# Optimization experiments

Hardware: AMD Instinct MI355X
Metric: run time of the kernel (lower is better)

The kernel has to match this reference:

```python
import jax, jax.numpy as jnp
import numpy as np
from jax import lax

# QKeras quantized_bits(8, 0, alpha=1, keep_negative=1):
#   delta = 2^-(bits-1) = 1/128, q(x) = clip(round(x*128), -128, 127)/128
QB_SCALE = 128.0
# QKeras quantized_relu(8, 0): q(x) = clip(round(x*256), 0, 255)/256
QR_SCALE = 256.0

def _ste(q, x):
    # straight-through estimator: forward = q(x), backward = identity
    return x + lax.stop_gradient(q - x)

def qbits(x):
    q = jnp.clip(jnp.round(x * QB_SCALE), -QB_SCALE, QB_SCALE - 1.0) / QB_SCALE
    return _ste(q, x)

def qrelu(x):
    q = jnp.clip(jnp.round(x * QR_SCALE), 0.0, QR_SCALE - 1.0) / QR_SCALE
    return _ste(q, x)


def setup_inputs() -> dict:
    key = jax.random.key(0)
    ks = jax.random.split(key, 9)
    B, C, F = 1000000, 16, 3
    dims = [C * F, 64, 32, 32]
    x = jax.random.normal(ks[0], (B, C, F), dtype=jnp.float32)
    def w(k, i, o):
        return jax.random.normal(k, (i, o), dtype=jnp.float32) * (0.5 / np.sqrt(i))
    inp = {"x": x}
    for li in range(3):
        inp[f"w{li+1}"] = w(ks[1 + 2 * li], dims[li], dims[li + 1])
        inp[f"b{li+1}"] = jax.random.normal(ks[2 + 2 * li], (dims[li + 1],), dtype=jnp.float32) * 0.05
    inp["wout"] = w(ks[7], dims[-1], 5)
    inp["bout"] = jax.random.normal(ks[8], (5,), dtype=jnp.float32) * 0.05
    return inp


def reference(x, w1, b1, w2, b2, w3, b3, wout, bout):
    h = x.reshape(x.shape[0], -1)  # Flatten: [B, 48]
    for w, b in ((w1, b1), (w2, b2), (w3, b3)):
        # QDense: fake-quantize kernel & bias, fp32 matmul, quantized_relu
        h = qrelu(h @ qbits(w) + qbits(b))
    return h @ wout + bout  # final float Dense -> logits [B, 5]
```

## Files before the change

kernel.cpp:

```cpp
#include <hip/hip_runtime.h>
#include <hip/hip_bf16.h>

typedef short  short8 __attribute__((ext_vector_type(8)));
typedef float  f32x4  __attribute__((ext_vector_type(4)));
typedef unsigned int u32;
typedef unsigned long long u64;
typedef unsigned short u16;

__device__ __forceinline__ u32 f2bf(float v) {
    u32 u = __float_as_uint(v);
    return (u + 0x7FFFu + ((u >> 16) & 1u)) >> 16;
}
__device__ __forceinline__ float qround128(float w) {
    float q = rintf(w * 128.0f);
    return fminf(fmaxf(q, -128.0f), 127.0f);
}
__device__ __forceinline__ u32 cvtpk(float a, float b) {
    __hip_bfloat162 h = __float22bfloat162_rn(make_float2(a, b));
    union { __hip_bfloat162 h; u32 u; } cv; cv.h = h; return cv.u;
}
__device__ __forceinline__ float q255(float v) {
    return fminf(fmaxf(rintf(v), 0.f), 255.f);
}
union FragU { short8 s; u32 u[4]; };
__device__ __forceinline__ short8 pack2(f32x4 a, f32x4 b) {
    FragU f;
    f.u[0] = cvtpk(q255(a[0]), q255(a[1]));
    f.u[1] = cvtpk(q255(a[2]), q255(a[3]));
    f.u[2] = cvtpk(q255(b[0]), q255(b[1]));
    f.u[3] = cvtpk(q255(b[2]), q255(b[3]));
    return f.s;
}
__device__ __forceinline__ f32x4 mfma16(short8 a, short8 b, f32x4 c) {
    return __builtin_amdgcn_mfma_f32_16x16x32_bf16(a, b, c, 0, 0, 0);
}


__global__ void prep(const float* __restrict__ w1, const float* __restrict__ b1,
                     const float* __restrict__ w2, const float* __restrict__ b2,
                     const float* __restrict__ w3, const float* __restrict__ b3,
                     const float* __restrict__ wo, const float* __restrict__ bo,
                     u16* __restrict__ wsh) {
    int idx = blockIdx.x * 256 + threadIdx.x;
    if (idx < 16 * 512) {
        int blk = idx >> 9, e = idx & 511;
        int l = e >> 3, j = e & 7;
        int r  = l & 15;
        int gi = l >> 4;
        int fp = 16 * (j >> 2) + 4 * gi + (j & 3);
        float val = 0.f;
        if (blk < 8) {
            int mt = blk >> 1, ks = blk & 1;
            int fo = mt * 16 + r;
            if (ks == 0) {
                val = 2.0f * qround128(w1[(12 * gi + j) * 64 + fo]);
            } else if (j < 4) {
                val = 2.0f * qround128(w1[(12 * gi + 8 + j) * 64 + fo]);
            } else if (gi == 3 && j == 7) {
                val = 2.0f * qround128(b1[fo]);
            }
        } else if (blk < 12) {
            int bi = blk - 8, mt = bi >> 1, ks = bi & 1;
            int f = ks * 32 + fp, fo = mt * 16 + r;
            val = qround128(w2[f * 32 + fo]) * (1.0f / 128.0f);
        } else if (blk < 14) {
            int mt = blk - 12;
            val = qround128(w3[fp * 32 + mt * 16 + r]) * (1.0f / 128.0f);
        } else {
            float wv = (r < 5) ? wo[fp * 5 + r] * (1.0f / 256.0f) : 0.f;
            u32 hb = f2bf(wv);
            if (blk == 14) { wsh[idx] = (u16)hb; return; }
            val = wv - __uint_as_float(hb << 16);
        }
        wsh[idx] = (u16)f2bf(val);
    }
    if (blockIdx.x == 0) {
        int t = threadIdx.x;
        float* wsf = (float*)(wsh + 8192);
        for (int i = t; i < 32; i += 256) wsf[64 + i]  = 2.0f * qround128(b2[i]);
        for (int i = t; i < 32; i += 256) wsf[96 + i]  = 2.0f * qround128(b3[i]);
        for (int i = t; i < 16; i += 256) wsf[128 + i] = (i < 5) ? bo[i] : 0.f;
    }
}


__global__ __launch_bounds__(256, 2) void mlp_mfma(const float* __restrict__ x,
                                                   const u16* __restrict__ wsh,
                                                   float* __restrict__ out, int ntiles) {
    const int tid = threadIdx.x;
    const int wid = tid >> 6, lane = tid & 63;
    const int c = lane & 15, g = lane >> 4;

    short8 wf[16];
    const short8* wv = (const short8*)wsh;
    #pragma unroll
    for (int i = 0; i < 16; ++i) wf[i] = wv[i * 64 + lane];

    const float* wsf = (const float*)(wsh + 8192);
    f32x4 b2q[2], b3q[2], boq;
    #pragma unroll
    for (int i = 0; i < 2; ++i) b2q[i] = *(const f32x4*)(wsf + 64 + i * 16 + 4 * g);
    #pragma unroll
    for (int i = 0; i < 2; ++i) b3q[i] = *(const f32x4*)(wsf + 96 + i * 16 + 4 * g);
    boq = *(const f32x4*)(wsf + 128 + 4 * g);

    const int xoff = c * 48 + g * 12;
    const int npacks = (ntiles + 3) >> 2;
    const int gw = blockIdx.x * 4 + wid;
    const int nw = gridDim.x * 4;
    const f32x4 zero4 = {0.f, 0.f, 0.f, 0.f};

    for (int p = gw; p < npacks; p += nw) {
        float4 xq0[4], xq1[4], xq2[4];
        #pragma unroll
        for (int i = 0; i < 4; ++i) {
            int t = 4 * p + i;
            int tl = (t < ntiles) ? t : (ntiles - 1);
            const float* xl = x + (size_t)tl * 768 + xoff;
            xq0[i] = *(const float4*)(xl);
            xq1[i] = *(const float4*)(xl + 4);
            xq2[i] = *(const float4*)(xl + 8);
        }

        #pragma unroll
        for (int i = 0; i < 4; ++i) {
            float v[12] = {xq0[i].x, xq0[i].y, xq0[i].z, xq0[i].w,
                           xq1[i].x, xq1[i].y, xq1[i].z, xq1[i].w,
                           xq2[i].x, xq2[i].y, xq2[i].z, xq2[i].w};
            FragU bh0, bl0, bh1, bl1;
            #pragma unroll
            for (int q = 0; q < 4; ++q) {
                u32 uu = cvtpk(v[2 * q], v[2 * q + 1]);
                bh0.u[q] = uu;
                float r0 = v[2 * q]     - __uint_as_float(uu << 16);
                float r1 = v[2 * q + 1] - __uint_as_float(uu & 0xFFFF0000u);
                bl0.u[q] = cvtpk(r0, r1);
            }
            #pragma unroll
            for (int q = 0; q < 2; ++q) {
                u32 uu = cvtpk(v[8 + 2 * q], v[9 + 2 * q]);
                bh1.u[q] = uu;
                float r0 = v[8 + 2 * q] - __uint_as_float(uu << 16);
                float r1 = v[9 + 2 * q] - __uint_as_float(uu & 0xFFFF0000u);
                bl1.u[q] = cvtpk(r0, r1);
            }
            bh1.u[2] = 0u;
            bh1.u[3] = (g == 3) ? 0x3F800000u : 0u;
            bl1.u[2] = 0u; bl1.u[3] = 0u;

            f32x4 acc1[4];
            #pragma unroll
            for (int mt = 0; mt < 4; ++mt) {
                f32x4 ah = mfma16(wf[mt * 2 + 0], bh0.s, zero4);
                ah = mfma16(wf[mt * 2 + 1], bh1.s, ah);
                f32x4 al = mfma16(wf[mt * 2 + 0], bl0.s, zero4);
                al = mfma16(wf[mt * 2 + 1], bl1.s, al);
                acc1[mt] = ah + al;
            }
            short8 p0 = pack2(acc1[0], acc1[1]);
            short8 p1 = pack2(acc1[2], acc1[3]);

            f32x4 a20 = mfma16(wf[8],  p0, b2q[0]);
            f32x4 a21 = mfma16(wf[9],  p1, zero4);
            f32x4 a22 = mfma16(wf[10], p0, b2q[1]);
            f32x4 a23 = mfma16(wf[11], p1, zero4);
            short8 p2 = pack2(a20 + a21, a22 + a23);

            f32x4 a30 = mfma16(wf[12], p2, b3q[0]);
            f32x4 a31 = mfma16(wf[13], p2, b3q[1]);
            short8 p3 = pack2(a30, a31);

            f32x4 aoh = mfma16(wf[14], p3, boq);
            f32x4 aol = mfma16(wf[15], p3, zero4);
            f32x4 ao = aoh + aol;

            int t = 4 * p + i;
            if (t < ntiles) {
                float* orow = out + (size_t)t * 80 + c * 5;
                if (g == 0) {
                    orow[0] = ao[0]; orow[1] = ao[1]; orow[2] = ao[2]; orow[3] = ao[3];
                } else if (g == 1) {
                    orow[4] = ao[0];
                }
            }
        }
    }
}

extern "C" void kernel_launch(void* const* d_in, const int* in_sizes, int n_in,
                              void* d_out, int out_size, void* d_ws, size_t ws_size,
                              hipStream_t stream) {
    const float* x  = (const float*)d_in[0];
    const float* w1 = (const float*)d_in[1];
    const float* b1 = (const float*)d_in[2];
    const float* w2 = (const float*)d_in[3];
    const float* b2 = (const float*)d_in[4];
    const float* w3 = (const float*)d_in[5];
    const float* b3 = (const float*)d_in[6];
    const float* wo = (const float*)d_in[7];
    const float* bo = (const float*)d_in[8];
    float* out = (float*)d_out;

    int B = in_sizes[0] / 48;
    int ntiles = B / 16;
    int npacks = (ntiles + 3) / 4;

    prep<<<32, 256, 0, stream>>>(w1, b1, w2, b2, w3, b3, wo, bo, (u16*)d_ws);

    int blocks = (npacks + 7) / 8;
    if (blocks > 2048) blocks = 2048;
    mlp_mfma<<<blocks, 256, 0, stream>>>(x, (const u16*)d_ws, out, ntiles);
}
```

Baseline: 51.74 us.

## Double-buffer input tiles into LDS with async global_load_lds per wave

Each wave now streams x directly into its own double-buffered LDS region with global_load_lds. It prefetches the next pack of two tiles while computing the current one, waiting on vmcnt instead of holding four tiles of loads in registers. Pack size drops from four tiles to two, the occupancy hint rises to 3 blocks per SM, and the grid size is recomputed to match. The four scalar output stores become one float4 store at an address that is not 16-byte aligned. The aim is better latency hiding on this memory-bound stream, at the cost of 48KB of LDS per block, hand-written waitcnt logic and an extra LDS read pass.

```diff
diff --git a/kernel.cpp b/kernel.cpp
--- a/kernel.cpp
+++ b/kernel.cpp
@@ -34,7 +34,12 @@
 __device__ __forceinline__ f32x4 mfma16(short8 a, short8 b, f32x4 c) {
     return __builtin_amdgcn_mfma_f32_16x16x32_bf16(a, b, c, 0, 0, 0);
 }
-
+__device__ __forceinline__ void gload16(const float* src, float* lds_dst) {
+    __builtin_amdgcn_global_load_lds(
+        (const __attribute__((address_space(1))) u32*)src,
+        (__attribute__((address_space(3))) u32*)lds_dst,
+        16, 0, 0);
+}
 
 __global__ void prep(const float* __restrict__ w1, const float* __restrict__ b1,
                      const float* __restrict__ w2, const float* __restrict__ b2,
@@ -84,9 +89,10 @@
 }
 
 
-__global__ __launch_bounds__(256, 2) void mlp_mfma(const float* __restrict__ x,
+__global__ __launch_bounds__(256, 3) void mlp_mfma(const float* __restrict__ x,
                                                    const u16* __restrict__ wsh,
                                                    float* __restrict__ out, int ntiles) {
+    __shared__ __align__(16) float smem[4][2][1536];
     const int tid = threadIdx.x;
     const int wid = tid >> 6, lane = tid & 63;
     const int c = lane & 15, g = lane >> 4;
@@ -104,29 +110,47 @@
     for (int i = 0; i < 2; ++i) b3q[i] = *(const f32x4*)(wsf + 96 + i * 16 + 4 * g);
     boq = *(const f32x4*)(wsf + 128 + 4 * g);
 
-    const int xoff = c * 48 + g * 12;
-    const int npacks = (ntiles + 3) >> 2;
+    const int npacks = (ntiles + 1) >> 1;
     const int gw = blockIdx.x * 4 + wid;
     const int nw = gridDim.x * 4;
     const f32x4 zero4 = {0.f, 0.f, 0.f, 0.f};
-
-    for (int p = gw; p < npacks; p += nw) {
-        float4 xq0[4], xq1[4], xq2[4];
+    const int roff = c * 48 + g * 12;
+
+    auto stage = [&](int buf, int pk) {
         #pragma unroll
-        for (int i = 0; i < 4; ++i) {
-            int t = 4 * p + i;
-            int tl = (t < ntiles) ? t : (ntiles - 1);
-            const float* xl = x + (size_t)tl * 768 + xoff;
-            xq0[i] = *(const float4*)(xl);
-            xq1[i] = *(const float4*)(xl + 4);
-            xq2[i] = *(const float4*)(xl + 8);
-        }
+        for (int s = 0; s < 6; ++s) {
+            int tt = 2 * pk + (s >= 3 ? 1 : 0);
+            if (tt >= ntiles) tt = ntiles - 1;
+            const float* src = x + (size_t)tt * 768 + (s % 3) * 256 + lane * 4;
+            gload16(src, &smem[wid][buf][s * 256]);
+        }
+    };
+
+    int p = gw;
+    int buf = 0;
+    if (p < npacks) stage(0, p);
+
+    for (; p < npacks; p += nw) {
+        const int pn = p + nw;
+        const bool have = pn < npacks;
+        if (have) {
+            stage(buf ^ 1, pn);
+            asm volatile("s_waitcnt vmcnt(6)" ::: "memory");
+        } else {
+            asm volatile("s_waitcnt vmcnt(0)" ::: "memory");
+        }
+        __builtin_amdgcn_sched_barrier(0);
 
         #pragma unroll
-        for (int i = 0; i < 4; ++i) {
-            float v[12] = {xq0[i].x, xq0[i].y, xq0[i].z, xq0[i].w,
-                           xq1[i].x, xq1[i].y, xq1[i].z, xq1[i].w,
-                           xq2[i].x, xq2[i].y, xq2[i].z, xq2[i].w};
+        for (int i = 0; i < 2; ++i) {
+            const float* T = &smem[wid][buf][i * 768];
+            float4 q0 = *(const float4*)(T + roff);
+            float4 q1 = *(const float4*)(T + roff + 4);
+            float4 q2 = *(const float4*)(T + roff + 8);
+            float v[12] = {q0.x, q0.y, q0.z, q0.w,
+                           q1.x, q1.y, q1.z, q1.w,
+                           q2.x, q2.y, q2.z, q2.w};
+
             FragU bh0, bl0, bh1, bl1;
             #pragma unroll
             for (int q = 0; q < 4; ++q) {
@@ -174,16 +198,17 @@
             f32x4 aol = mfma16(wf[15], p3, zero4);
             f32x4 ao = aoh + aol;
 
-            int t = 4 * p + i;
+            int t = 2 * p + i;
             if (t < ntiles) {
                 float* orow = out + (size_t)t * 80 + c * 5;
                 if (g == 0) {
-                    orow[0] = ao[0]; orow[1] = ao[1]; orow[2] = ao[2]; orow[3] = ao[3];
+                    *(float4*)orow = make_float4(ao[0], ao[1], ao[2], ao[3]);
                 } else if (g == 1) {
                     orow[4] = ao[0];
                 }
             }
         }
+        buf ^= 1;
     }
 }
 
@@ -203,11 +228,11 @@
 
     int B = in_sizes[0] / 48;
     int ntiles = B / 16;
-    int npacks = (ntiles + 3) / 4;
+    int npacks = (ntiles + 1) / 2;
 
     prep<<<32, 256, 0, stream>>>(w1, b1, w2, b2, w3, b3, wo, bo, (u16*)d_ws);
 
-    int blocks = (npacks + 7) / 8;
+    int blocks = (npacks + 3) / 4;
     if (blocks > 2048) blocks = 2048;
     mlp_mfma<<<blocks, 256, 0, stream>>>(x, (const u16*)d_ws, out, ntiles);
 }
```

Result: no change. 51.40 us (median of 2 runs) (-0.7%).

## Software-pipeline x loads with nontemporal prefetch double-buffer and fixed grid

Applied to the files above, without the earlier changes.

Restructures the main loop into a two-tile-per-pack ping-pong. The next pack's inputs are issued as nontemporal global loads (inline asm with explicit vmcnt waits) while the current pack is computed. This is meant to hide global load latency behind the MFMA chain. The grid is fixed at 512 blocks, and the output store for the first four logits becomes a float4 store, which assumes aligned addresses. It also drops odd-tile handling: npacks = ntiles/2 truncates, so an odd tile count would be silently skipped, and the hand-written waitcnt relies on compiler scheduling staying as expected.

```diff
diff --git a/kernel.cpp b/kernel.cpp
--- a/kernel.cpp
+++ b/kernel.cpp
@@ -34,7 +34,11 @@
 __device__ __forceinline__ f32x4 mfma16(short8 a, short8 b, f32x4 c) {
     return __builtin_amdgcn_mfma_f32_16x16x32_bf16(a, b, c, 0, 0, 0);
 }
-
+__device__ __forceinline__ f32x4 ldnt(const float* p) {
+    f32x4 r;
+    asm volatile("global_load_dwordx4 %0, %1, off nt" : "=&v"(r) : "v"(p) : "memory");
+    return r;
+}
 
 __global__ void prep(const float* __restrict__ w1, const float* __restrict__ b1,
                      const float* __restrict__ w2, const float* __restrict__ b2,
@@ -105,85 +109,114 @@
     boq = *(const f32x4*)(wsf + 128 + 4 * g);
 
     const int xoff = c * 48 + g * 12;
-    const int npacks = (ntiles + 3) >> 2;
+    const int npacks = ntiles >> 1;
     const int gw = blockIdx.x * 4 + wid;
     const int nw = gridDim.x * 4;
     const f32x4 zero4 = {0.f, 0.f, 0.f, 0.f};
 
-    for (int p = gw; p < npacks; p += nw) {
-        float4 xq0[4], xq1[4], xq2[4];
+    auto do_tile = [&](f32x4 qa, f32x4 qb, f32x4 qc, int t) {
+        float v[12] = {qa[0], qa[1], qa[2], qa[3],
+                       qb[0], qb[1], qb[2], qb[3],
+                       qc[0], qc[1], qc[2], qc[3]};
+        FragU bh0, bl0, bh1, bl1;
         #pragma unroll
-        for (int i = 0; i < 4; ++i) {
-            int t = 4 * p + i;
-            int tl = (t < ntiles) ? t : (ntiles - 1);
-            const float* xl = x + (size_t)tl * 768 + xoff;
-            xq0[i] = *(const float4*)(xl);
-            xq1[i] = *(const float4*)(xl + 4);
-            xq2[i] = *(const float4*)(xl + 8);
-        }
-
+        for (int q = 0; q < 4; ++q) {
+            u32 uu = cvtpk(v[2 * q], v[2 * q + 1]);
+            bh0.u[q] = uu;
+            float r0 = v[2 * q]     - __uint_as_float(uu << 16);
+            float r1 = v[2 * q + 1] - __uint_as_float(uu & 0xFFFF0000u);
+            bl0.u[q] = cvtpk(r0, r1);
+        }
         #pragma unroll
-        for (int i = 0; i < 4; ++i) {
-            float v[12] = {xq0[i].x, xq0[i].y, xq0[i].z, xq0[i].w,
-                           xq1[i].x, xq1[i].y, xq1[i].z, xq1[i].w,
-                           xq2[i].x, xq2[i].y, xq2[i].z, xq2[i].w};
-            FragU bh0, bl0, bh1, bl1;
-            #pragma unroll
-            for (int q = 0; q < 4; ++q) {
-                u32 uu = cvtpk(v[2 * q], v[2 * q + 1]);
-                bh0.u[q] = uu;
-                float r0 = v[2 * q]     - __uint_as_float(uu << 16);
-                float r1 = v[2 * q + 1] - __uint_as_float(uu & 0xFFFF0000u);
-                bl0.u[q] = cvtpk(r0, r1);
-            }
-            #pragma unroll
-            for (int q = 0; q < 2; ++q) {
-                u32 uu = cvtpk(v[8 + 2 * q], v[9 + 2 * q]);
-                bh1.u[q] = uu;
-                float r0 = v[8 + 2 * q] - __uint_as_float(uu << 16);
-                float r1 = v[9 + 2 * q] - __uint_as_float(uu & 0xFFFF0000u);
-                bl1.u[q] = cvtpk(r0, r1);
-            }
-            bh1.u[2] = 0u;
-            bh1.u[3] = (g == 3) ? 0x3F800000u : 0u;
-            bl1.u[2] = 0u; bl1.u[3] = 0u;
-
-            f32x4 acc1[4];
-            #pragma unroll
-            for (int mt = 0; mt < 4; ++mt) {
-                f32x4 ah = mfma16(wf[mt * 2 + 0], bh0.s, zero4);
-                ah = mfma16(wf[mt * 2 + 1], bh1.s, ah);
-                f32x4 al = mfma16(wf[mt * 2 + 0], bl0.s, zero4);
-                al = mfma16(wf[mt * 2 + 1], bl1.s, al);
-                acc1[mt] = ah + al;
-            }
-            short8 p0 = pack2(acc1[0], acc1[1]);
-            short8 p1 = pack2(acc1[2], acc1[3]);
-
-            f32x4 a20 = mfma16(wf[8],  p0, b2q[0]);
-            f32x4 a21 = mfma16(wf[9],  p1, zero4);
-            f32x4 a22 = mfma16(wf[10], p0, b2q[1]);
-            f32x4 a23 = mfma16(wf[11], p1, zero4);
-            short8 p2 = pack2(a20 + a21, a22 + a23);
-
-            f32x4 a30 = mfma16(wf[12], p2, b3q[0]);
-            f32x4 a31 = mfma16(wf[13], p2, b3q[1]);
-            short8 p3 = pack2(a30, a31);
-
-            f32x4 aoh = mfma16(wf[14], p3, boq);
-            f32x4 aol = mfma16(wf[15], p3, zero4);
-            f32x4 ao = aoh + aol;
-
-            int t = 4 * p + i;
-            if (t < ntiles) {
-                float* orow = out + (size_t)t * 80 + c * 5;
-                if (g == 0) {
-                    orow[0] = ao[0]; orow[1] = ao[1]; orow[2] = ao[2]; orow[3] = ao[3];
-                } else if (g == 1) {
-                    orow[4] = ao[0];
-                }
-            }
-        }
+        for (int q = 0; q < 2; ++q) {
+            u32 uu = cvtpk(v[8 + 2 * q], v[9 + 2 * q]);
+            bh1.u[q] = uu;
+            float r0 = v[8 + 2 * q] - __uint_as_float(uu << 16);
+            float r1 = v[9 + 2 * q] - __uint_as_float(uu & 0xFFFF0000u);
+            bl1.u[q] = cvtpk(r0, r1);
+        }
+        bh1.u[2] = 0u;
+        bh1.u[3] = (g == 3) ? 0x3F800000u : 0u;
+        bl1.u[2] = 0u; bl1.u[3] = 0u;
+
+        f32x4 acc1[4];
+        #pragma unroll
+        for (int mt = 0; mt < 4; ++mt) {
+            f32x4 ah = mfma16(wf[mt * 2 + 0], bh0.s, zero4);
+            ah = mfma16(wf[mt * 2 + 1], bh1.s, ah);
+            f32x4 al = mfma16(wf[mt * 2 + 0], bl0.s, zero4);
+            al = mfma16(wf[mt * 2 + 1], bl1.s, al);
+            acc1[mt] = ah + al;
+        }
+        short8 p0 = pack2(acc1[0], acc1[1]);
+        short8 p1 = pack2(acc1[2], acc1[3]);
+
+        f32x4 a20 = mfma16(wf[8],  p0, b2q[0]);
+        f32x4 a21 = mfma16(wf[9],  p1, zero4);
+        f32x4 a22 = mfma16(wf[10], p0, b2q[1]);
+        f32x4 a23 = mfma16(wf[11], p1, zero4);
+        short8 p2 = pack2(a20 + a21, a22 + a23);
+
+        f32x4 a30 = mfma16(wf[12], p2, b3q[0]);
+        f32x4 a31 = mfma16(wf[13], p2, b3q[1]);
+        short8 p3 = pack2(a30, a31);
+
+        f32x4 aoh = mfma16(wf[14], p3, boq);
+        f32x4 aol = mfma16(wf[15], p3, zero4);
+        f32x4 ao = aoh + aol;
+
+        float* orow = out + (size_t)t * 80 + c * 5;
+        if (g == 0) {
+            *(float4*)orow = make_float4(ao[0], ao[1], ao[2], ao[3]);
+        } else if (g == 1) {
+            orow[4] = ao[0];
+        }
+    };
+
+    int p = gw;
+    if (p >= npacks) return;
+
+    f32x4 A0, A1, A2, A3, A4, A5, B0, B1, B2, B3, B4, B5;
+    {
+        const float* t0 = x + (size_t)(2 * p) * 768 + xoff;
+        const float* t1 = x + (size_t)(2 * p + 1) * 768 + xoff;
+        A0 = ldnt(t0); A1 = ldnt(t0 + 4); A2 = ldnt(t0 + 8);
+        A3 = ldnt(t1); A4 = ldnt(t1 + 4); A5 = ldnt(t1 + 8);
+    }
+
+    for (;;) {
+        int pn = p + nw;
+        bool haveB = pn < npacks;
+        if (haveB) {
+            const float* t0 = x + (size_t)(2 * pn) * 768 + xoff;
+            const float* t1 = x + (size_t)(2 * pn + 1) * 768 + xoff;
+            B0 = ldnt(t0); B1 = ldnt(t0 + 4); B2 = ldnt(t0 + 8);
+            B3 = ldnt(t1); B4 = ldnt(t1 + 4); B5 = ldnt(t1 + 8);
+            asm volatile("s_waitcnt vmcnt(6)" ::: "memory");
+        } else {
+            asm volatile("s_waitcnt vmcnt(0)" ::: "memory");
+        }
+        __builtin_amdgcn_sched_barrier(0);
+        do_tile(A0, A1, A2, 2 * p);
+        do_tile(A3, A4, A5, 2 * p + 1);
+        if (!haveB) break;
+
+        int p2 = pn + nw;
+        bool haveA = p2 < npacks;
+        if (haveA) {
+            const float* t0 = x + (size_t)(2 * p2) * 768 + xoff;
+            const float* t1 = x + (size_t)(2 * p2 + 1) * 768 + xoff;
+            A0 = ldnt(t0); A1 = ldnt(t0 + 4); A2 = ldnt(t0 + 8);
+            A3 = ldnt(t1); A4 = ldnt(t1 + 4); A5 = ldnt(t1 + 8);
+            asm volatile("s_waitcnt vmcnt(6)" ::: "memory");
+        } else {
+            asm volatile("s_waitcnt vmcnt(0)" ::: "memory");
+        }
+        __builtin_amdgcn_sched_barrier(0);
+        do_tile(B0, B1, B2, 2 * pn);
+        do_tile(B3, B4, B5, 2 * pn + 1);
+        if (!haveA) break;
+        p = p2;
     }
 }
 
@@ -203,11 +236,8 @@
 
     int B = in_sizes[0] / 48;
     int ntiles = B / 16;
-    int npacks = (ntiles + 3) / 4;
 
     prep<<<32, 256, 0, stream>>>(w1, b1, w2, b2, w3, b3, wo, bo, (u16*)d_ws);
 
-    int blocks = (npacks + 7) / 8;
-    if (blocks > 2048) blocks = 2048;
-    mlp_mfma<<<blocks, 256, 0, stream>>>(x, (const u16*)d_ws, out, ntiles);
-}
+    mlp_mfma<<<512, 256, 0, stream>>>(x, (const u16*)d_ws, out, ntiles);
+}
```

After: 64.34 us. 24.4% more time.
